# Optimization experiments

Measured on AMD Instinct MI355X. Metric: run time of the kernel, lower is better.

The kernel has to match this reference:

```python
import jax, jax.numpy as jnp
import numpy as np

N_NODES = 50000
IN_CH = 128
DIM = 32
HEADS = 8
OUT_CH = 2
NEG_SLOPE = 0.2


def _glorot(key, shape):
    fan_in = shape[0]
    return jax.random.normal(key, shape, dtype=jnp.float32) / jnp.sqrt(jnp.float32(fan_in))


def gatv2_conv(x, Wl, bl, Wr, br, att, bias, src, dst, n_nodes, heads, out_c, concat):
    """PyG GATv2Conv (eval mode, add_self_loops already applied to src/dst)."""
    xl = (x @ Wl + bl).reshape(n_nodes, heads, out_c)  # [N,H,C] source transform
    xr = (x @ Wr + br).reshape(n_nodes, heads, out_c)  # [N,H,C] target transform
    # per-edge GATv2 score: a^T LeakyReLU(xl[j] + xr[i])
    e = jax.nn.leaky_relu(xl[src] + xr[dst], NEG_SLOPE)          # [E,H,C]
    score = jnp.einsum('ehc,hc->eh', e, att)                      # [E,H]
    # segment softmax over incoming edges of each target node
    smax = jax.ops.segment_max(score, dst, num_segments=n_nodes)  # [N,H]
    ex = jnp.exp(score - smax[dst])
    denom = jax.ops.segment_sum(ex, dst, num_segments=n_nodes)
    alpha = ex / (denom[dst] + 1e-16)                             # [E,H]
    out = jax.ops.segment_sum(alpha[:, :, None] * xl[src], dst, num_segments=n_nodes)  # [N,H,C]
    if concat:
        out = out.reshape(n_nodes, heads * out_c)
    else:
        out = out.mean(axis=1)
    return out + bias


def setup_inputs() -> dict:
    key = jax.random.key(0)
    ks = jax.random.split(key, 20)
    x = jax.random.normal(ks[0], (N_NODES, IN_CH), dtype=jnp.float32)
    edge_index = jax.random.randint(ks[1], (2, 400000), 0, N_NODES, dtype=jnp.int32)
    H, C = HEADS, DIM
    hid = H * C  # 256
    params = {
        'Wl1': _glorot(ks[2], (IN_CH, hid)), 'bl1': jnp.zeros((hid,), jnp.float32),
        'Wr1': _glorot(ks[3], (IN_CH, hid)), 'br1': jnp.zeros((hid,), jnp.float32),
        'att1': _glorot(ks[4], (H, C)), 'b1': jnp.zeros((hid,), jnp.float32),
        'Wl3': _glorot(ks[5], (hid, hid)), 'bl3': jnp.zeros((hid,), jnp.float32),
        'Wr3': _glorot(ks[6], (hid, hid)), 'br3': jnp.zeros((hid,), jnp.float32),
        'att3': _glorot(ks[7], (H, C)), 'b3': jnp.zeros((hid,), jnp.float32),
        'Wl2': _glorot(ks[8], (hid, OUT_CH)), 'bl2': jnp.zeros((OUT_CH,), jnp.float32),
        'Wr2': _glorot(ks[9], (hid, OUT_CH)), 'br2': jnp.zeros((OUT_CH,), jnp.float32),
        'att2': _glorot(ks[10], (1, OUT_CH)), 'b2': jnp.zeros((OUT_CH,), jnp.float32),
    }
    return {'x': x, 'edge_index': edge_index, **params}


def reference(x, edge_index, Wl1, bl1, Wr1, br1, att1, b1,
              Wl3, bl3, Wr3, br3, att3, b3,
              Wl2, bl2, Wr2, br2, att2, b2):
    n = x.shape[0]
    loop = jnp.arange(n, dtype=edge_index.dtype)
    src = jnp.concatenate([edge_index[0], loop])  # PyG add_self_loops
    dst = jnp.concatenate([edge_index[1], loop])
    # dropout layers are no-ops in eval mode
    h = jax.nn.elu(gatv2_conv(x, Wl1, bl1, Wr1, br1, att1, b1, src, dst, n, HEADS, DIM, True))
    h = jax.nn.elu(gatv2_conv(h, Wl3, bl3, Wr3, br3, att3, b3, src, dst, n, HEADS, DIM, True))
    h = gatv2_conv(h, Wl2, bl2, Wr2, br2, att2, b2, src, dst, n, 1, OUT_CH, False)
    return jax.nn.log_softmax(h, axis=-1)
```

## Files before the change

kernel.cpp:

```cpp
#include <hip/hip_runtime.h>
#include <cstdint>
#include <cstddef>


typedef __attribute__((ext_vector_type(8))) _Float16 v8h;
typedef __attribute__((ext_vector_type(2))) _Float16 h2;
typedef __attribute__((ext_vector_type(2))) __fp16 h2r;
typedef __attribute__((ext_vector_type(4))) float v4f;

__device__ __forceinline__ float lrelu(float v) { return fmaxf(v, 0.2f * v); }
__device__ __forceinline__ float elu1(float v)  { return v > 0.f ? v : expm1f(v); }

__device__ __forceinline__ unsigned short f2h(float f) {
  _Float16 h = (_Float16)f;
  return __builtin_bit_cast(unsigned short, h);
}
__device__ __forceinline__ float h2f(unsigned short s) {
  return (float)__builtin_bit_cast(_Float16, s);
}

__device__ __forceinline__ h2 cvt_pk(float a, float b) {
  h2r t = __builtin_amdgcn_cvt_pkrtz(a, b);
  return __builtin_bit_cast(h2, t);
}
__device__ __forceinline__ h2 pk2(float a) { return cvt_pk(a, a); }

__device__ __forceinline__ h2 lrelu_pk(h2 v) {
  unsigned int u = __builtin_bit_cast(unsigned int, v) & 0x7FFF7FFFu;
  h2 av = __builtin_bit_cast(h2, u);
  h2 c6 = {(_Float16)0.6f, (_Float16)0.6f};
  h2 c4 = {(_Float16)0.4f, (_Float16)0.4f};
  return v * c6 + av * c4;
}

__device__ __forceinline__ float dot2(h2 a, h2 b, float c) {
#if __has_builtin(__builtin_amdgcn_fdot2)
  return __builtin_amdgcn_fdot2(__builtin_bit_cast(h2r, a),
                                __builtin_bit_cast(h2r, b), c, false);
#else
  return fmaf((float)a[0], (float)b[0], fmaf((float)a[1], (float)b[1], c));
#endif
}

__device__ __forceinline__ void gl_lds16(const void* g, void* l) {
  __builtin_amdgcn_global_load_lds(
      (const __attribute__((address_space(1))) unsigned int*)g,
      (__attribute__((address_space(3))) unsigned int*)l, 16, 0, 0);
}


__global__ void k_count(const int* __restrict__ dst, int* __restrict__ deg, int E) {
  int e = blockIdx.x * blockDim.x + threadIdx.x;
  if (e < E) atomicAdd(&deg[dst[e]], 1);
}

__global__ __launch_bounds__(256) void k_bsum(const int* __restrict__ deg, int n,
                                              int* __restrict__ bsum) {
  __shared__ int red[256];
  int t = threadIdx.x, bid = blockIdx.x;
  int i0 = bid * 1024 + t * 4;
  int s = 0;
  if (i0 + 3 < n) {
    int4 v = *(const int4*)&deg[i0];
    s = v.x + v.y + v.z + v.w;
  } else {
#pragma unroll
    for (int j = 0; j < 4; ++j)
      if (i0 + j < n) s += deg[i0 + j];
  }
  red[t] = s;
  __syncthreads();
  for (int off = 128; off > 0; off >>= 1) {
    if (t < off) red[t] += red[t + off];
    __syncthreads();
  }
  if (t == 0) bsum[bid] = red[0];
}

__global__ __launch_bounds__(256) void k_offsets(const int* __restrict__ deg,
                                                 const int* __restrict__ bsum,
                                                 int nb, int n,
                                                 int* __restrict__ offs,
                                                 int* __restrict__ cursor) {
  __shared__ int sc[256];
  int t = threadIdx.x, bid = blockIdx.x;
  int base = 0;
  for (int b = 0; b < bid; ++b) base += bsum[b];
  int i0 = bid * 1024 + t * 4;
  int v0 = 0, v1 = 0, v2 = 0, v3 = 0;
  if (i0 + 3 < n) {
    int4 v = *(const int4*)&deg[i0];
    v0 = v.x; v1 = v.y; v2 = v.z; v3 = v.w;
  } else {
    if (i0 < n)     v0 = deg[i0];
    if (i0 + 1 < n) v1 = deg[i0 + 1];
    if (i0 + 2 < n) v2 = deg[i0 + 2];
    if (i0 + 3 < n) v3 = deg[i0 + 3];
  }
  int s = v0 + v1 + v2 + v3;
  sc[t] = s;
  __syncthreads();
  for (int off = 1; off < 256; off <<= 1) {
    int x = (t >= off) ? sc[t - off] : 0;
    __syncthreads();
    sc[t] += x;
    __syncthreads();
  }
  int run = base + sc[t] - s;
  int o0 = run, o1 = run + v0, o2 = o1 + v1, o3 = o2 + v2;
  if (i0 + 3 < n) {
    *(int4*)&offs[i0] = make_int4(o0, o1, o2, o3);
    *(int4*)&cursor[i0] = make_int4(o0, o1, o2, o3);
  } else {
    if (i0 < n)     { offs[i0] = o0;     cursor[i0] = o0; }
    if (i0 + 1 < n) { offs[i0 + 1] = o1; cursor[i0 + 1] = o1; }
    if (i0 + 2 < n) { offs[i0 + 2] = o2; cursor[i0 + 2] = o2; }
    if (i0 + 3 < n) { offs[i0 + 3] = o3; cursor[i0 + 3] = o3; }
  }
  if (bid == nb - 1 && t == 255) offs[n] = base + sc[255];
}

__global__ void k_scatter(const int* __restrict__ src, const int* __restrict__ dst,
                          int* __restrict__ cursor, int* __restrict__ csr_src, int E) {
  int e = blockIdx.x * blockDim.x + threadIdx.x;
  if (e < E) {
    int pos = atomicAdd(&cursor[dst[e]], 1);
    csr_src[pos] = src[e];
  }
}


__global__ void k_split(const float* __restrict__ Wl, const float* __restrict__ Wr,
                        int K, int logK, unsigned short* __restrict__ Bt) {
  int idx = blockIdx.x * blockDim.x + threadIdx.x;
  if (idx >= 512 * K) return;
  int n = idx >> logK;
  int k = idx & (K - 1);
  float w = (n < 256) ? Wl[(size_t)k * 256 + n] : Wr[(size_t)k * 256 + (n - 256)];
  Bt[idx] = f2h(w);
}


__global__ void k_quantA(const float* __restrict__ X, int Nreal, int total4,
                         unsigned short* __restrict__ Hh) {
  int idx = blockIdx.x * blockDim.x + threadIdx.x;
  if (idx >= total4) return;
  int row = idx >> 5;
  ushort4 uh;
  if (row < Nreal) {
    float4 v = *(const float4*)&X[(size_t)idx * 4];
    uh.x = f2h(v.x); uh.y = f2h(v.y); uh.z = f2h(v.z); uh.w = f2h(v.w);
  } else {
    uh = make_ushort4(0, 0, 0, 0);
  }
  *(ushort4*)&Hh[(size_t)idx * 4] = uh;
}


__global__ __launch_bounds__(256) void k_gemm_mfma(
    const unsigned short* __restrict__ A_g,
    int Nreal, int K,
    const unsigned short* __restrict__ Bt,
    const float* __restrict__ bl, const float* __restrict__ br,
    unsigned short* __restrict__ xl_h, unsigned short* __restrict__ xr_h) {
  __shared__ __align__(16) short Ah[64 * 32];
  __shared__ __align__(16) short Bh[256 * 32];

  const int tid = threadIdx.x;
  const int lane = tid & 63;
  const int wid = tid >> 6;
  const int l15 = lane & 15, g = lane >> 4;
  const int bm = blockIdx.x * 64;
  const int half = blockIdx.y;
  const int bn = half * 256;

  v4f acc[4][4];
#pragma unroll
  for (int m = 0; m < 4; ++m)
#pragma unroll
    for (int n = 0; n < 4; ++n) acc[m][n] = (v4f)(0.f);

  const int arow = tid >> 2, aslot = tid & 3;
  const int aoct = aslot ^ ((arow >> 1) & 3);
  const size_t gaBase = (size_t)(bm + arow) * K + aoct * 8;
  short* AhW = Ah + wid * 512;

  for (int k0 = 0; k0 < K; k0 += 32) {
    gl_lds16(A_g + gaBase + k0, AhW);
#pragma unroll
    for (int it = 0; it < 4; ++it) {
      int task = it * 256 + tid;
      int col = task >> 2, slot = task & 3;
      int oct = slot ^ ((col >> 1) & 3);
      size_t gb = (size_t)(bn + col) * K + k0 + oct * 8;
      gl_lds16(Bt + gb, Bh + it * 2048 + wid * 512);
    }
    __syncthreads();

    v8h a_h[4], b_h[4];
#pragma unroll
    for (int m = 0; m < 4; ++m) {
      int r = m * 16 + l15;
      int s = g ^ ((r >> 1) & 3);
      a_h[m] = *(const v8h*)&Ah[r * 32 + s * 8];
    }
#pragma unroll
    for (int n = 0; n < 4; ++n) {
      int c = wid * 64 + n * 16 + l15;
      int s = g ^ ((c >> 1) & 3);
      b_h[n] = *(const v8h*)&Bh[c * 32 + s * 8];
    }
#pragma unroll
    for (int m = 0; m < 4; ++m)
#pragma unroll
      for (int n = 0; n < 4; ++n)
        acc[m][n] = __builtin_amdgcn_mfma_f32_16x16x32_f16(a_h[m], b_h[n], acc[m][n], 0, 0, 0);
    __syncthreads();
  }

  float* scr = (float*)Bh + wid * 320;
  const int erow = lane >> 2, ecq = lane & 3;
  unsigned short* outp = half ? xr_h : xl_h;
  const float* bias = half ? br : bl;
#pragma unroll
  for (int m = 0; m < 4; ++m) {
#pragma unroll
    for (int n = 0; n < 4; ++n) {
#pragma unroll
      for (int r = 0; r < 4; ++r) scr[(g * 4 + r) * 20 + l15] = acc[m][n][r];
      float4 v = *(const float4*)&scr[erow * 20 + ecq * 4];
      int row = bm + m * 16 + erow;
      if (row < Nreal) {
        int col = wid * 64 + n * 16 + ecq * 4;
        float4 bv = *(const float4*)&bias[col];
        ushort4 u;
        u.x = f2h(v.x + bv.x); u.y = f2h(v.y + bv.y);
        u.z = f2h(v.z + bv.z); u.w = f2h(v.w + bv.w);
        *(ushort4*)&outp[(size_t)row * 256 + col] = u;
      }
    }
  }
}


__global__ __launch_bounds__(256) void k_edge(
    const unsigned short* __restrict__ xl_h,
    const unsigned short* __restrict__ xr_h,
    const int* __restrict__ offs, const int* __restrict__ csr_src,
    const float* __restrict__ att,
    const float* __restrict__ bias,
    unsigned short* __restrict__ hout,
    int n) {
  int lane = threadIdx.x & 63;
  int node = blockIdx.x * (blockDim.x >> 6) + (threadIdx.x >> 6);
  if (node >= n) return;

  float4 attf = *(const float4*)&att[lane * 4];
  h2 atta = cvt_pk(attf.x, attf.y);
  h2 attb = cvt_pk(attf.z, attf.w);
  uint2 urx = *(const uint2*)&xr_h[(size_t)node * 256 + lane * 4];
  h2 xra = __builtin_bit_cast(h2, urx.x), xrb = __builtin_bit_cast(h2, urx.y);

  uint2 us = *(const uint2*)&xl_h[(size_t)node * 256 + lane * 4];
  h2 acca = __builtin_bit_cast(h2, us.x), accb = __builtin_bit_cast(h2, us.y);
  float p = dot2(lrelu_pk(acca + xra), atta, 0.f);
  p = dot2(lrelu_pk(accb + xrb), attb, p);
  p += __shfl_xor(p, 1);
  p += __shfl_xor(p, 2);
  p += __shfl_xor(p, 4);
  float m = p, d = 1.f;

  int e0 = offs[node], e1 = offs[node + 1];
  int e = e0;
  for (; e + 1 < e1; e += 2) {
    int j1 = csr_src[e], j2 = csr_src[e + 1];
    uint2 u1 = *(const uint2*)&xl_h[(size_t)j1 * 256 + lane * 4];
    uint2 u2 = *(const uint2*)&xl_h[(size_t)j2 * 256 + lane * 4];
    h2 x1a = __builtin_bit_cast(h2, u1.x), x1b = __builtin_bit_cast(h2, u1.y);
    h2 x2a = __builtin_bit_cast(h2, u2.x), x2b = __builtin_bit_cast(h2, u2.y);
    float p1 = dot2(lrelu_pk(x1a + xra), atta, 0.f);
    p1 = dot2(lrelu_pk(x1b + xrb), attb, p1);
    float p2 = dot2(lrelu_pk(x2a + xra), atta, 0.f);
    p2 = dot2(lrelu_pk(x2b + xrb), attb, p2);
    p1 += __shfl_xor(p1, 1); p2 += __shfl_xor(p2, 1);
    p1 += __shfl_xor(p1, 2); p2 += __shfl_xor(p2, 2);
    p1 += __shfl_xor(p1, 4); p2 += __shfl_xor(p2, 4);
    float m12 = fmaxf(p1, p2);
    float w1 = __expf(p1 - m12), w2 = __expf(p2 - m12);
    float d12 = w1 + w2;
    h2 w1p = pk2(w1), w2p = pk2(w2);
    h2 ca = x1a * w1p + x2a * w2p;
    h2 cb = x1b * w1p + x2b * w2p;
    float mN = fmaxf(m, m12);
    float r  = __expf(m - mN);
    float r2 = __expf(m12 - mN);
    d = fmaf(d, r, d12 * r2);
    h2 rp = pk2(r), r2p = pk2(r2);
    acca = acca * rp + ca * r2p;
    accb = accb * rp + cb * r2p;
    m = mN;
  }
  if (e < e1) {
    int j = csr_src[e];
    uint2 u = *(const uint2*)&xl_h[(size_t)j * 256 + lane * 4];
    h2 xa = __builtin_bit_cast(h2, u.x), xb = __builtin_bit_cast(h2, u.y);
    float p1 = dot2(lrelu_pk(xa + xra), atta, 0.f);
    p1 = dot2(lrelu_pk(xb + xrb), attb, p1);
    p1 += __shfl_xor(p1, 1);
    p1 += __shfl_xor(p1, 2);
    p1 += __shfl_xor(p1, 4);
    float mN = fmaxf(m, p1);
    float r = __expf(m - mN), w1 = __expf(p1 - mN);
    d = fmaf(d, r, w1);
    h2 rp = pk2(r), w1p = pk2(w1);
    acca = acca * rp + xa * w1p;
    accb = accb * rp + xb * w1p;
  }

  float inv = 1.f / (d + 1e-16f);
  float4 b4 = *(const float4*)&bias[lane * 4];
  float o0 = elu1(fmaf((float)acca[0], inv, b4.x));
  float o1 = elu1(fmaf((float)acca[1], inv, b4.y));
  float o2 = elu1(fmaf((float)accb[0], inv, b4.z));
  float o3 = elu1(fmaf((float)accb[1], inv, b4.w));
  ushort4 uo;
  uo.x = f2h(o0); uo.y = f2h(o1); uo.z = f2h(o2); uo.w = f2h(o3);
  *(ushort4*)&hout[(size_t)node * 256 + lane * 4] = uo;
}


__global__ __launch_bounds__(256) void k_lin3(
    const unsigned short* __restrict__ hq,
    const float* __restrict__ Wl, const float* __restrict__ bl,
    const float* __restrict__ Wr, const float* __restrict__ br,
    float* __restrict__ xlr3,
    int n) {
  int lane = threadIdx.x & 63;
  int node = blockIdx.x * (blockDim.x >> 6) + (threadIdx.x >> 6);
  if (node >= n) return;
  ushort4 uh = *(const ushort4*)&hq[(size_t)node * 256 + lane * 4];
  float hv[4] = {h2f(uh.x), h2f(uh.y), h2f(uh.z), h2f(uh.w)};
  float al0 = 0.f, al1 = 0.f, ar0 = 0.f, ar1 = 0.f;
#pragma unroll
  for (int j = 0; j < 4; ++j) {
    int k = lane * 4 + j;
    al0 = fmaf(hv[j], Wl[k * 2 + 0], al0);
    al1 = fmaf(hv[j], Wl[k * 2 + 1], al1);
    ar0 = fmaf(hv[j], Wr[k * 2 + 0], ar0);
    ar1 = fmaf(hv[j], Wr[k * 2 + 1], ar1);
  }
#pragma unroll
  for (int s = 1; s < 64; s <<= 1) {
    al0 += __shfl_xor(al0, s);
    al1 += __shfl_xor(al1, s);
    ar0 += __shfl_xor(ar0, s);
    ar1 += __shfl_xor(ar1, s);
  }
  if (lane == 0) {
    float4 o = make_float4(al0 + bl[0], al1 + bl[1], ar0 + br[0], ar1 + br[1]);
    *(float4*)&xlr3[(size_t)node * 4] = o;
  }
}


__global__ void k_edge3(const float* __restrict__ xlr3,
                        const int* __restrict__ offs, const int* __restrict__ csr_src,
                        const float* __restrict__ att,
                        const float* __restrict__ b,
                        float* __restrict__ out, int n) {
  int i = blockIdx.x * blockDim.x + threadIdx.x;
  if (i >= n) return;
  float a0 = att[0], a1 = att[1];
  float xr0 = xlr3[(size_t)i * 4 + 2], xr1 = xlr3[(size_t)i * 4 + 3];
  float sl0 = xlr3[(size_t)i * 4 + 0], sl1 = xlr3[(size_t)i * 4 + 1];
  float m = lrelu(sl0 + xr0) * a0 + lrelu(sl1 + xr1) * a1;
  float d = 1.f, ac0 = sl0, ac1 = sl1;
  int e0 = offs[i], e1 = offs[i + 1];
  for (int e = e0; e < e1; ++e) {
    int j = csr_src[e];
    float xl0 = xlr3[(size_t)j * 4 + 0], xl1 = xlr3[(size_t)j * 4 + 1];
    float p = lrelu(xl0 + xr0) * a0 + lrelu(xl1 + xr1) * a1;
    float mN = fmaxf(m, p);
    float r = __expf(m - mN), w = __expf(p - mN);
    d = fmaf(d, r, w);
    ac0 = fmaf(ac0, r, w * xl0);
    ac1 = fmaf(ac1, r, w * xl1);
    m = mN;
  }
  float inv = 1.f / (d + 1e-16f);
  float o0 = fmaf(ac0, inv, b[0]);
  float o1 = fmaf(ac1, inv, b[1]);
  float mx = fmaxf(o0, o1);
  float lse = mx + logf(expf(o0 - mx) + expf(o1 - mx));
  out[(size_t)i * 2 + 0] = o0 - lse;
  out[(size_t)i * 2 + 1] = o1 - lse;
}


static inline size_t align_up(size_t v, size_t a) { return (v + a - 1) & ~(a - 1); }

extern "C" void kernel_launch(void* const* d_in, const int* in_sizes, int n_in,
                              void* d_out, int out_size, void* d_ws, size_t ws_size,
                              hipStream_t stream) {
  const float* x    = (const float*)d_in[0];
  const int*   ei   = (const int*)d_in[1];
  const float* Wl1  = (const float*)d_in[2];
  const float* bl1  = (const float*)d_in[3];
  const float* Wr1  = (const float*)d_in[4];
  const float* br1  = (const float*)d_in[5];
  const float* att1 = (const float*)d_in[6];
  const float* b1   = (const float*)d_in[7];
  const float* Wl3  = (const float*)d_in[8];
  const float* bl3  = (const float*)d_in[9];
  const float* Wr3  = (const float*)d_in[10];
  const float* br3  = (const float*)d_in[11];
  const float* att3 = (const float*)d_in[12];
  const float* b3   = (const float*)d_in[13];
  const float* Wl2  = (const float*)d_in[14];
  const float* bl2  = (const float*)d_in[15];
  const float* Wr2  = (const float*)d_in[16];
  const float* br2  = (const float*)d_in[17];
  const float* att2 = (const float*)d_in[18];
  const float* b2   = (const float*)d_in[19];

  const int N = in_sizes[0] / 128;
  const int E = in_sizes[1] / 2;
  const int Npad = ((N + 63) / 64) * 64;
  const int* srcp = ei;
  const int* dstp = ei + E;

  char* w = (char*)d_ws;
  size_t off = 0;
  int* deg     = (int*)(w + off); off = align_up(off + (size_t)N * 4, 256);
  int* offs    = (int*)(w + off); off = align_up(off + (size_t)(N + 1) * 4, 256);
  int* cursor  = (int*)(w + off); off = align_up(off + (size_t)N * 4, 256);
  int* csr_src = (int*)(w + off); off = align_up(off + (size_t)E * 4, 256);
  int* bsum    = (int*)(w + off); off = align_up(off + (size_t)256 * 4, 256);
  unsigned short* x_h  = (unsigned short*)(w + off); off = align_up(off + (size_t)Npad * 128 * 2, 256);
  unsigned short* h_h  = (unsigned short*)(w + off); off = align_up(off + (size_t)Npad * 256 * 2, 256);
  unsigned short* xlh  = (unsigned short*)(w + off); off = align_up(off + (size_t)N * 256 * 2, 256);
  unsigned short* xrh  = (unsigned short*)(w + off); off = align_up(off + (size_t)N * 256 * 2, 256);
  float* xlr3  = (float*)(w + off); off = align_up(off + (size_t)N * 4 * 4, 256);
  unsigned short* Bt1 = (unsigned short*)(w + off); off = align_up(off + (size_t)512 * 128 * 2, 256);
  unsigned short* Bt2 = (unsigned short*)(w + off); off = align_up(off + (size_t)512 * 256 * 2, 256);
  (void)ws_size;

  const int nb = (N + 1023) / 1024;

  hipMemsetAsync(deg, 0, (size_t)N * 4, stream);
  k_count<<<(E + 255) / 256, 256, 0, stream>>>(dstp, deg, E);
  k_bsum<<<nb, 256, 0, stream>>>(deg, N, bsum);
  k_offsets<<<nb, 256, 0, stream>>>(deg, bsum, nb, N, offs, cursor);
  k_scatter<<<(E + 255) / 256, 256, 0, stream>>>(srcp, dstp, cursor, csr_src, E);

  k_split<<<(512 * 128 + 255) / 256, 256, 0, stream>>>(Wl1, Wr1, 128, 7, Bt1);
  k_split<<<(512 * 256 + 255) / 256, 256, 0, stream>>>(Wl3, Wr3, 256, 8, Bt2);
  {
    int total4 = Npad * 128 / 4;
    k_quantA<<<(total4 + 255) / 256, 256, 0, stream>>>(x, N, total4, x_h);
  }
  hipMemsetAsync(h_h + (size_t)N * 256, 0, (size_t)(Npad - N) * 256 * 2, stream);

  dim3 ggrid(Npad / 64, 2);
  int nodeBlocks = (N + 3) / 4;

  k_gemm_mfma<<<ggrid, 256, 0, stream>>>(x_h, N, 128, Bt1, bl1, br1, xlh, xrh);
  k_edge<<<nodeBlocks, 256, 0, stream>>>(xlh, xrh, offs, csr_src, att1, b1, h_h, N);

  k_gemm_mfma<<<ggrid, 256, 0, stream>>>(h_h, N, 256, Bt2, bl3, br3, xlh, xrh);
  k_edge<<<nodeBlocks, 256, 0, stream>>>(xlh, xrh, offs, csr_src, att3, b3, h_h, N);

  k_lin3<<<nodeBlocks, 256, 0, stream>>>(h_h, Wl2, bl2, Wr2, br2, xlr3, N);
  k_edge3<<<(N + 255) / 256, 256, 0, stream>>>(xlr3, offs, csr_src, att2, b2,
                                               (float*)d_out, N);
}
```

Baseline: 249.3 us.

## Double-buffer GEMM LDS staging and use 32-bit index math in edge kernels

The MFMA GEMM now double-buffers its A and B LDS tiles. It issues the next k-tile's global-to-LDS loads before computing the current one and waits with explicit vmcnt counts and raw s_barrier instead of __syncthreads. Separately, the edge, lin3 and GEMM kernels switch from size_t to unsigned 32-bit offset arithmetic to cut 64-bit address computation in the gather loops. The changes double the GEMM's LDS footprint, which may lower occupancy. The hand-coded vmcnt value assumes exactly five outstanding loads per stage.

```diff
diff --git a/kernel.cpp b/kernel.cpp
--- a/kernel.cpp
+++ b/kernel.cpp
@@ -163,8 +163,8 @@
     const unsigned short* __restrict__ Bt,
     const float* __restrict__ bl, const float* __restrict__ br,
     unsigned short* __restrict__ xl_h, unsigned short* __restrict__ xr_h) {
-  __shared__ __align__(16) short Ah[64 * 32];
-  __shared__ __align__(16) short Bh[256 * 32];
+  __shared__ __align__(16) short Ah[2][64 * 32];
+  __shared__ __align__(16) short Bh[2][256 * 32];
 
   const int tid = threadIdx.x;
   const int lane = tid & 63;
@@ -182,43 +182,55 @@
 
   const int arow = tid >> 2, aslot = tid & 3;
   const int aoct = aslot ^ ((arow >> 1) & 3);
-  const size_t gaBase = (size_t)(bm + arow) * K + aoct * 8;
-  short* AhW = Ah + wid * 512;
-
-  for (int k0 = 0; k0 < K; k0 += 32) {
-    gl_lds16(A_g + gaBase + k0, AhW);
+  const unsigned gaBase = (unsigned)(bm + arow) * K + aoct * 8;
+
+  auto STAGE = [&](int buf, int k0) {
+    gl_lds16(A_g + (gaBase + k0), &Ah[buf][wid * 512]);
 #pragma unroll
     for (int it = 0; it < 4; ++it) {
       int task = it * 256 + tid;
       int col = task >> 2, slot = task & 3;
       int oct = slot ^ ((col >> 1) & 3);
-      size_t gb = (size_t)(bn + col) * K + k0 + oct * 8;
-      gl_lds16(Bt + gb, Bh + it * 2048 + wid * 512);
+      unsigned gb = (unsigned)(bn + col) * K + k0 + oct * 8;
+      gl_lds16(Bt + gb, &Bh[buf][it * 2048 + wid * 512]);
     }
-    __syncthreads();
+  };
+
+  const int nt = K >> 5;
+  STAGE(0, 0);
+  for (int t = 0; t < nt; ++t) {
+    const int cur = t & 1;
+    if (t + 1 < nt) {
+      STAGE(cur ^ 1, (t + 1) << 5);
+      asm volatile("s_waitcnt vmcnt(5)" ::: "memory");
+    } else {
+      asm volatile("s_waitcnt vmcnt(0)" ::: "memory");
+    }
+    __builtin_amdgcn_sched_barrier(0);
+    __builtin_amdgcn_s_barrier();
 
     v8h a_h[4], b_h[4];
 #pragma unroll
     for (int m = 0; m < 4; ++m) {
       int r = m * 16 + l15;
       int s = g ^ ((r >> 1) & 3);
-      a_h[m] = *(const v8h*)&Ah[r * 32 + s * 8];
+      a_h[m] = *(const v8h*)&Ah[cur][r * 32 + s * 8];
     }
 #pragma unroll
     for (int n = 0; n < 4; ++n) {
       int c = wid * 64 + n * 16 + l15;
       int s = g ^ ((c >> 1) & 3);
-      b_h[n] = *(const v8h*)&Bh[c * 32 + s * 8];
+      b_h[n] = *(const v8h*)&Bh[cur][c * 32 + s * 8];
     }
 #pragma unroll
     for (int m = 0; m < 4; ++m)
 #pragma unroll
       for (int n = 0; n < 4; ++n)
         acc[m][n] = __builtin_amdgcn_mfma_f32_16x16x32_f16(a_h[m], b_h[n], acc[m][n], 0, 0, 0);
-    __syncthreads();
-  }
-
-  float* scr = (float*)Bh + wid * 320;
+    __builtin_amdgcn_s_barrier();
+  }
+
+  float* scr = (float*)&Bh[0][0] + wid * 320;
   const int erow = lane >> 2, ecq = lane & 3;
   unsigned short* outp = half ? xr_h : xl_h;
   const float* bias = half ? br : bl;
@@ -255,13 +267,15 @@
   int node = blockIdx.x * (blockDim.x >> 6) + (threadIdx.x >> 6);
   if (node >= n) return;
 
-  float4 attf = *(const float4*)&att[lane * 4];
+  const unsigned lb = (unsigned)(lane << 2);
+  float4 attf = *(const float4*)&att[lb];
   h2 atta = cvt_pk(attf.x, attf.y);
   h2 attb = cvt_pk(attf.z, attf.w);
-  uint2 urx = *(const uint2*)&xr_h[(size_t)node * 256 + lane * 4];
+  const unsigned noff = ((unsigned)node << 8) + lb;
+  uint2 urx = *(const uint2*)(xr_h + noff);
   h2 xra = __builtin_bit_cast(h2, urx.x), xrb = __builtin_bit_cast(h2, urx.y);
 
-  uint2 us = *(const uint2*)&xl_h[(size_t)node * 256 + lane * 4];
+  uint2 us = *(const uint2*)(xl_h + noff);
   h2 acca = __builtin_bit_cast(h2, us.x), accb = __builtin_bit_cast(h2, us.y);
   float p = dot2(lrelu_pk(acca + xra), atta, 0.f);
   p = dot2(lrelu_pk(accb + xrb), attb, p);
@@ -274,8 +288,8 @@
   int e = e0;
   for (; e + 1 < e1; e += 2) {
     int j1 = csr_src[e], j2 = csr_src[e + 1];
-    uint2 u1 = *(const uint2*)&xl_h[(size_t)j1 * 256 + lane * 4];
-    uint2 u2 = *(const uint2*)&xl_h[(size_t)j2 * 256 + lane * 4];
+    uint2 u1 = *(const uint2*)(xl_h + (((unsigned)j1 << 8) + lb));
+    uint2 u2 = *(const uint2*)(xl_h + (((unsigned)j2 << 8) + lb));
     h2 x1a = __builtin_bit_cast(h2, u1.x), x1b = __builtin_bit_cast(h2, u1.y);
     h2 x2a = __builtin_bit_cast(h2, u2.x), x2b = __builtin_bit_cast(h2, u2.y);
     float p1 = dot2(lrelu_pk(x1a + xra), atta, 0.f);
@@ -302,7 +316,7 @@
   }
   if (e < e1) {
     int j = csr_src[e];
-    uint2 u = *(const uint2*)&xl_h[(size_t)j * 256 + lane * 4];
+    uint2 u = *(const uint2*)(xl_h + (((unsigned)j << 8) + lb));
     h2 xa = __builtin_bit_cast(h2, u.x), xb = __builtin_bit_cast(h2, u.y);
     float p1 = dot2(lrelu_pk(xa + xra), atta, 0.f);
     p1 = dot2(lrelu_pk(xb + xrb), attb, p1);
@@ -318,14 +332,14 @@
   }
 
   float inv = 1.f / (d + 1e-16f);
-  float4 b4 = *(const float4*)&bias[lane * 4];
+  float4 b4 = *(const float4*)&bias[lb];
   float o0 = elu1(fmaf((float)acca[0], inv, b4.x));
   float o1 = elu1(fmaf((float)acca[1], inv, b4.y));
   float o2 = elu1(fmaf((float)accb[0], inv, b4.z));
   float o3 = elu1(fmaf((float)accb[1], inv, b4.w));
   ushort4 uo;
   uo.x = f2h(o0); uo.y = f2h(o1); uo.z = f2h(o2); uo.w = f2h(o3);
-  *(ushort4*)&hout[(size_t)node * 256 + lane * 4] = uo;
+  *(ushort4*)(hout + noff) = uo;
 }
 
 
@@ -338,7 +352,7 @@
   int lane = threadIdx.x & 63;
   int node = blockIdx.x * (blockDim.x >> 6) + (threadIdx.x >> 6);
   if (node >= n) return;
-  ushort4 uh = *(const ushort4*)&hq[(size_t)node * 256 + lane * 4];
+  ushort4 uh = *(const ushort4*)(hq + (((unsigned)node << 8) + (lane << 2)));
   float hv[4] = {h2f(uh.x), h2f(uh.y), h2f(uh.z), h2f(uh.w)};
   float al0 = 0.f, al1 = 0.f, ar0 = 0.f, ar1 = 0.f;
 #pragma unroll
```

After: 240.6 us. 3.5% less time.
